# Optimization experiments

Hardware: AMD Instinct MI355X
Metric: run time of the kernel (lower is better)

## Reference

```python
import jax, jax.numpy as jnp
import numpy as np

B, D = 512, 512

def setup_inputs() -> dict:
    key = jax.random.key(0)
    k1, k2, k3, k4 = jax.random.split(key, 4)
    return {
        "img_proj": jax.random.normal(k1, (B, D), dtype=jnp.float32),
        "audio_proj": jax.random.normal(k2, (B, D), dtype=jnp.float32),
        "W": jax.random.normal(k3, (D, D), dtype=jnp.float32) * 0.02,
        "b": jax.random.normal(k4, (D,), dtype=jnp.float32) * 0.02,
    }

def reference(img_proj, audio_proj, W, b):
    # concat of raw projections (saved before img_proj is transformed)
    concat_proj = jnp.concatenate([img_proj, audio_proj], axis=-1)  # [B, 2D]
    # linear + tanh on image projection
    img_t = jnp.tanh(img_proj @ W.T + b)                            # [B, D]
    # rank-1 bilinear co-attention map: L[b,i,j] = img_t[b,i] * audio[b,j]
    L = img_t[:, :, None] * audio_proj[:, None, :]                  # [B, D, D]
    # softmax over dim=1 (rows), attend audio: C_img[b,e] = sum_d audio[b,d] * S1[b,e,d]
    S1 = jax.nn.softmax(L, axis=1)
    C_img = jnp.einsum('bd,bed->be', audio_proj, S1)                # [B, D]
    # softmax over dim=2 (cols), attend tanh-image: C_audio[b,e] = sum_d img_t[b,d] * S2[b,d,e]
    S2 = jax.nn.softmax(L, axis=2)
    C_audio = jnp.einsum('bd,bde->be', img_t, S2)                   # [B, D]
    fused = jnp.concatenate([C_img, C_audio], axis=-1)              # [B, 2D]
    return jnp.concatenate([concat_proj, fused], axis=-1)           # [B, 4D]
```

## Files before the change

kernel.cpp:

```cpp
#include <hip/hip_runtime.h>

#define K_TERMS 24

#define INVF_INIT { \
  1.0f, 1.0f, 0.5f, 1.6666666666666666e-01f, 4.1666666666666664e-02f, \
  8.3333333333333332e-03f, 1.3888888888888889e-03f, 1.9841269841269841e-04f, \
  2.4801587301587302e-05f, 2.7557319223985893e-06f, 2.7557319223985888e-07f, \
  2.5052108385441720e-08f, 2.0876756987868098e-09f, 1.6059043836821613e-10f, \
  1.1470745597729725e-11f, 7.6471637318198164e-13f, 4.7794773323873852e-14f, \
  2.8114572543455206e-15f, 1.5619206968586225e-16f, 8.2206352466243295e-18f, \
  4.1103176233121648e-19f, 1.9572941063391263e-20f, 8.8967913924505741e-22f, \
  3.8681701706306835e-23f }

typedef __attribute__((ext_vector_type(4))) float floatx4;
typedef __attribute__((ext_vector_type(8))) short short8;

__device__ __forceinline__ unsigned short f2bf_rn(float f) {
  union { float f; unsigned u; } v; v.f = f;
  const unsigned r = v.u + 0x7FFFu + ((v.u >> 16) & 1u);
  return (unsigned short)(r >> 16);
}

__global__ __launch_bounds__(256) void gemm_tanh_mfma(
    const float* __restrict__ img, const float* __restrict__ W,
    const float* __restrict__ bias, float* __restrict__ tdst, int tstride) {
  __shared__ unsigned short Abf[32][40];
  __shared__ unsigned short Wbf[32][40];
  const int tid = threadIdx.x;
  const int bx = blockIdx.x;
  const int by = blockIdx.y;
  const int r  = tid >> 3;
  const int c4 = (tid & 7) * 4;
  const int lane = tid & 63;
  const int wv = tid >> 6;
  const int bm = (wv >> 1) * 16;
  const int en = (wv & 1) * 16;
  const int frow = lane & 15;
  const int kg = lane >> 4;

  floatx4 acc = {0.f, 0.f, 0.f, 0.f};
  const float* aprow = img + (size_t)(by * 32 + r) * 512;
  const float* wprow = W   + (size_t)(bx * 32 + r) * 512;

  for (int k0 = 0; k0 < 512; k0 += 32) {
    const float4 av = *(const float4*)(aprow + k0 + c4);
    const float4 wl = *(const float4*)(wprow + k0 + c4);
    __syncthreads();
    ushort4 ab, wb;
    ab.x = f2bf_rn(av.x); ab.y = f2bf_rn(av.y);
    ab.z = f2bf_rn(av.z); ab.w = f2bf_rn(av.w);
    wb.x = f2bf_rn(wl.x); wb.y = f2bf_rn(wl.y);
    wb.z = f2bf_rn(wl.z); wb.w = f2bf_rn(wl.w);
    *(ushort4*)&Abf[r][c4] = ab;
    *(ushort4*)&Wbf[r][c4] = wb;
    __syncthreads();
    const short8 afrag = *(const short8*)&Abf[bm + frow][kg * 8];
    const short8 wfrag = *(const short8*)&Wbf[en + frow][kg * 8];
    acc = __builtin_amdgcn_mfma_f32_16x16x32_bf16(afrag, wfrag, acc, 0, 0, 0);
  }

  const int e = bx * 32 + en + frow;
  const float bv = bias[e];
  const int b_base = by * 32 + bm + kg * 4;
#pragma unroll
  for (int i = 0; i < 4; ++i) {
    tdst[(size_t)(b_base + i) * tstride + e] = tanhf(acc[i] + bv);
  }
}

__global__ __launch_bounds__(512) void coattn_moments(
    const float* __restrict__ img, const float* __restrict__ audio,
    const float* __restrict__ tsrc, int tstride, float* __restrict__ out) {
  const int tid = threadIdx.x;
  const int b0 = blockIdx.x * 2;

  __shared__ float aL[2][512];
  __shared__ float tL[2][512];
  __shared__ float cwL[2][512];
  __shared__ float rwL[2][512];
  __shared__ float gT[2][K_TERMS], gA[2][K_TERMS];
  __shared__ float gS[2][K_TERMS], gR[2][K_TERMS];

  constexpr float INVF[K_TERMS] = INVF_INIT;

#pragma unroll
  for (int s = tid; s < 1024; s += 512) {
    const int r = s >> 9, i = s & 511;
    const float iv = img[(size_t)(b0 + r) * 512 + i];
    const float av = audio[(size_t)(b0 + r) * 512 + i];
    out[(size_t)(b0 + r) * 2048 + i] = iv;
    out[(size_t)(b0 + r) * 2048 + 512 + i] = av;
    aL[r][i] = av;
    tL[r][i] = tsrc[(size_t)(b0 + r) * tstride + i];
  }
  __syncthreads();

  const int wave = tid >> 6, lane = tid & 63;

  if (wave < 4) {
    const int r = wave >> 1, typ = wave & 1;
    const float* src = typ ? aL[r] : tL[r];
    float part[K_TERMS];
#pragma unroll
    for (int k = 0; k < K_TERMS; ++k) part[k] = 0.f;
#pragma unroll
    for (int u = 0; u < 8; ++u) {
      const float x = src[lane + 64 * u];
      float p = x;
      part[1] += p;
#pragma unroll
      for (int k = 2; k < K_TERMS; ++k) { p *= x; part[k] += p; }
    }
#pragma unroll
    for (int m = 1; m < 64; m <<= 1) {
#pragma unroll
      for (int k = 1; k < K_TERMS; ++k) part[k] += __shfl_xor(part[k], m, 64);
    }
    if (lane == 0) {
      float* g = typ ? gA[r] : gT[r];
      g[0] = 512.0f;
#pragma unroll
      for (int k = 1; k < K_TERMS; ++k) g[k] = part[k] * INVF[k];
    }
  }
  __syncthreads();

  {
    const int grp = tid >> 7, e0 = tid & 127;
    const int r = grp >> 1, kind = grp & 1;
    float g[K_TERMS];
    const float* gsrc = kind ? gA[r] : gT[r];
#pragma unroll
    for (int k = 0; k < K_TERMS; ++k) g[k] = gsrc[k];
    const float* xs = kind ? tL[r] : aL[r];
    float* dst = kind ? rwL[r] : cwL[r];
#pragma unroll
    for (int u = 0; u < 4; ++u) {
      const int e = e0 + 128 * u;
      const float x = xs[e];
      float s = g[K_TERMS - 1];
#pragma unroll
      for (int k = K_TERMS - 2; k >= 0; --k) s = fmaf(s, x, g[k]);
      dst[e] = x / s;
    }
  }
  __syncthreads();

  if (wave < 4) {
    const int r = wave >> 1, typ = wave & 1;
    const float* xs = typ ? tL[r] : aL[r];
    const float* ws = typ ? rwL[r] : cwL[r];
    float part[K_TERMS];
#pragma unroll
    for (int k = 0; k < K_TERMS; ++k) part[k] = 0.f;
#pragma unroll
    for (int u = 0; u < 8; ++u) {
      const int i = lane + 64 * u;
      const float x = xs[i];
      float p = ws[i];
      part[0] += p;
#pragma unroll
      for (int k = 1; k < K_TERMS; ++k) { p *= x; part[k] += p; }
    }
#pragma unroll
    for (int m = 1; m < 64; m <<= 1) {
#pragma unroll
      for (int k = 0; k < K_TERMS; ++k) part[k] += __shfl_xor(part[k], m, 64);
    }
    if (lane == 0) {
      float* g = typ ? gR[r] : gS[r];
#pragma unroll
      for (int k = 0; k < K_TERMS; ++k) g[k] = part[k] * INVF[k];
    }
  }
  __syncthreads();

  {
    const int grp = tid >> 7, e0 = tid & 127;
    const int r = grp >> 1, kind = grp & 1;
    float g[K_TERMS];
    const float* gsrc = kind ? gR[r] : gS[r];
#pragma unroll
    for (int k = 0; k < K_TERMS; ++k) g[k] = gsrc[k];
    const float* xs = kind ? aL[r] : tL[r];
    float* op = out + (size_t)(b0 + r) * 2048 + 1024 + kind * 512;
#pragma unroll
    for (int u = 0; u < 4; ++u) {
      const int e = e0 + 128 * u;
      const float x = xs[e];
      float s = g[K_TERMS - 1];
#pragma unroll
      for (int k = K_TERMS - 2; k >= 0; --k) s = fmaf(s, x, g[k]);
      op[e] = s;
    }
  }
}

extern "C" void kernel_launch(void* const* d_in, const int* in_sizes, int n_in,
                              void* d_out, int out_size, void* d_ws, size_t ws_size,
                              hipStream_t stream) {
  const float* img   = (const float*)d_in[0];
  const float* audio = (const float*)d_in[1];
  const float* W     = (const float*)d_in[2];
  const float* bias  = (const float*)d_in[3];
  float* out = (float*)d_out;

  float* tdst;
  int tstride;
  if (ws_size >= (size_t)(512 * 512 * 4)) {
    tdst = (float*)d_ws;
    tstride = 512;
  } else {
    tdst = out + 1024;
    tstride = 2048;
  }

  hipLaunchKernelGGL(gemm_tanh_mfma, dim3(16, 16), dim3(256), 0, stream,
                     img, W, bias, tdst, tstride);
  hipLaunchKernelGGL(coattn_moments, dim3(256), dim3(512), 0, stream,
                     img, audio, tdst, tstride, out);
}
```

Baseline: 76.25 us.

## Load GEMM fragments directly from global with register prefetch, drop LDS staging

The GEMM kernel no longer stages bf16 tiles through shared memory with two barriers per k-step. Each lane now loads its own MFMA fragment straight from global memory as float4 pairs. A four-deep register ring prefetches the next k-slices while the current one is packed to bf16 and fed to MFMA. This removes the synchronisation and LDS round trips, at the cost of more registers and less coalesced global loads.

```diff
diff --git a/kernel.cpp b/kernel.cpp
--- a/kernel.cpp
+++ b/kernel.cpp
@@ -15,56 +15,67 @@
 typedef __attribute__((ext_vector_type(4))) float floatx4;
 typedef __attribute__((ext_vector_type(8))) short short8;
 
-__device__ __forceinline__ unsigned short f2bf_rn(float f) {
+__device__ __forceinline__ unsigned f2bf_rn(float f) {
   union { float f; unsigned u; } v; v.f = f;
-  const unsigned r = v.u + 0x7FFFu + ((v.u >> 16) & 1u);
-  return (unsigned short)(r >> 16);
-}
-
-__global__ __launch_bounds__(256) void gemm_tanh_mfma(
+  return (v.u + 0x7FFFu + ((v.u >> 16) & 1u)) >> 16;
+}
+__device__ __forceinline__ unsigned pk_bf(float lo, float hi) {
+  return (f2bf_rn(lo) & 0xFFFFu) | (f2bf_rn(hi) << 16);
+}
+
+union S8 { short8 s; unsigned u[4]; };
+
+__global__ __launch_bounds__(256) void gemm_tanh_direct(
     const float* __restrict__ img, const float* __restrict__ W,
     const float* __restrict__ bias, float* __restrict__ tdst, int tstride) {
-  __shared__ unsigned short Abf[32][40];
-  __shared__ unsigned short Wbf[32][40];
   const int tid = threadIdx.x;
   const int bx = blockIdx.x;
   const int by = blockIdx.y;
-  const int r  = tid >> 3;
-  const int c4 = (tid & 7) * 4;
-  const int lane = tid & 63;
-  const int wv = tid >> 6;
-  const int bm = (wv >> 1) * 16;
-  const int en = (wv & 1) * 16;
+  const int wv = tid >> 6, lane = tid & 63;
   const int frow = lane & 15;
   const int kg = lane >> 4;
+  const int brow = by * 32 + (wv >> 1) * 16 + frow;
+  const int erow = bx * 32 + (wv & 1) * 16 + frow;
+
+  const float* ap = img + (size_t)brow * 512 + kg * 8;
+  const float* wp = W   + (size_t)erow * 512 + kg * 8;
 
   floatx4 acc = {0.f, 0.f, 0.f, 0.f};
-  const float* aprow = img + (size_t)(by * 32 + r) * 512;
-  const float* wprow = W   + (size_t)(bx * 32 + r) * 512;
-
-  for (int k0 = 0; k0 < 512; k0 += 32) {
-    const float4 av = *(const float4*)(aprow + k0 + c4);
-    const float4 wl = *(const float4*)(wprow + k0 + c4);
-    __syncthreads();
-    ushort4 ab, wb;
-    ab.x = f2bf_rn(av.x); ab.y = f2bf_rn(av.y);
-    ab.z = f2bf_rn(av.z); ab.w = f2bf_rn(av.w);
-    wb.x = f2bf_rn(wl.x); wb.y = f2bf_rn(wl.y);
-    wb.z = f2bf_rn(wl.z); wb.w = f2bf_rn(wl.w);
-    *(ushort4*)&Abf[r][c4] = ab;
-    *(ushort4*)&Wbf[r][c4] = wb;
-    __syncthreads();
-    const short8 afrag = *(const short8*)&Abf[bm + frow][kg * 8];
-    const short8 wfrag = *(const short8*)&Wbf[en + frow][kg * 8];
-    acc = __builtin_amdgcn_mfma_f32_16x16x32_bf16(afrag, wfrag, acc, 0, 0, 0);
-  }
-
-  const int e = bx * 32 + en + frow;
-  const float bv = bias[e];
-  const int b_base = by * 32 + bm + kg * 4;
+  float4 a0[4], a1[4], w0[4], w1[4];
+#pragma unroll
+  for (int s = 0; s < 4; ++s) {
+    a0[s] = *(const float4*)(ap + s * 32);
+    a1[s] = *(const float4*)(ap + s * 32 + 4);
+    w0[s] = *(const float4*)(wp + s * 32);
+    w1[s] = *(const float4*)(wp + s * 32 + 4);
+  }
+#pragma unroll
+  for (int ks = 0; ks < 16; ++ks) {
+    const int sl = ks & 3;
+    S8 af, wf;
+    af.u[0] = pk_bf(a0[sl].x, a0[sl].y);
+    af.u[1] = pk_bf(a0[sl].z, a0[sl].w);
+    af.u[2] = pk_bf(a1[sl].x, a1[sl].y);
+    af.u[3] = pk_bf(a1[sl].z, a1[sl].w);
+    wf.u[0] = pk_bf(w0[sl].x, w0[sl].y);
+    wf.u[1] = pk_bf(w0[sl].z, w0[sl].w);
+    wf.u[2] = pk_bf(w1[sl].x, w1[sl].y);
+    wf.u[3] = pk_bf(w1[sl].z, w1[sl].w);
+    acc = __builtin_amdgcn_mfma_f32_16x16x32_bf16(af.s, wf.s, acc, 0, 0, 0);
+    if (ks < 12) {
+      a0[sl] = *(const float4*)(ap + (ks + 4) * 32);
+      a1[sl] = *(const float4*)(ap + (ks + 4) * 32 + 4);
+      w0[sl] = *(const float4*)(wp + (ks + 4) * 32);
+      w1[sl] = *(const float4*)(wp + (ks + 4) * 32 + 4);
+    }
+  }
+
+  const int ecol = bx * 32 + (wv & 1) * 16 + frow;
+  const float bv = bias[ecol];
+  const int bbase = by * 32 + (wv >> 1) * 16 + kg * 4;
 #pragma unroll
   for (int i = 0; i < 4; ++i) {
-    tdst[(size_t)(b_base + i) * tstride + e] = tanhf(acc[i] + bv);
+    tdst[(size_t)(bbase + i) * tstride + ecol] = tanhf(acc[i] + bv);
   }
 }
 
@@ -215,7 +226,7 @@
     tstride = 2048;
   }
 
-  hipLaunchKernelGGL(gemm_tanh_mfma, dim3(16, 16), dim3(256), 0, stream,
+  hipLaunchKernelGGL(gemm_tanh_direct, dim3(16, 16), dim3(256), 0, stream,
                      img, W, bias, tdst, tstride);
   hipLaunchKernelGGL(coattn_moments, dim3(256), dim3(512), 0, stream,
                      img, audio, tdst, tstride, out);
```

New measurement: 81.32 us. 6.6% more time.
